# Performance work log

Hardware: AMD Instinct MI355X
Metric: run time of the kernel (lower is better)

Reference implementation:

```python
import jax, jax.numpy as jnp
import numpy as np

B, S, C = 4, 2048, 1024
E, H = 1024, 16
D = E // H  # head_dim = 64


def setup_inputs() -> dict:
    key = jax.random.key(0)
    k1, k2, k3, k4, k5 = jax.random.split(key, 5)
    s = 1.0 / np.sqrt(C)
    return {
        "x": jax.random.normal(k1, (B, S, C), dtype=jnp.float32),
        "w_qkv": jax.random.uniform(k2, (C, 3 * E), minval=-s, maxval=s, dtype=jnp.float32),
        "b_qkv": jax.random.uniform(k3, (3 * E,), minval=-s, maxval=s, dtype=jnp.float32),
        "w_out": jax.random.uniform(k4, (E, E), minval=-1.0 / np.sqrt(E), maxval=1.0 / np.sqrt(E), dtype=jnp.float32),
        "b_out": jax.random.uniform(k5, (E,), minval=-1.0 / np.sqrt(E), maxval=1.0 / np.sqrt(E), dtype=jnp.float32),
    }


def reference(x, w_qkv, b_qkv, w_out, b_out):
    b, s, _ = x.shape
    qkv = x @ w_qkv + b_qkv                      # [B,S,3E]
    qkv = qkv.reshape(b, s, 3, H, D)
    q = qkv[:, :, 0].transpose(0, 2, 1, 3)       # [B,H,S,D]
    k = qkv[:, :, 1].transpose(0, 2, 1, 3)
    v = qkv[:, :, 2].transpose(0, 2, 1, 3)
    scale = jnp.asarray(D, x.dtype) ** 0.5
    scores = jnp.einsum("bhqd,bhkd->bhqk", q, k) / scale
    attn = jax.nn.softmax(scores, axis=-1)       # dropout is identity in eval mode
    out = jnp.einsum("bhqk,bhkd->bhqd", attn, v)
    out = out.transpose(0, 2, 1, 3).reshape(b, s, E)
    return out @ w_out + b_out
```

## Files before the change

kernel.cpp:

```cpp
#include <hip/hip_runtime.h>


typedef _Float16 f16;
typedef f16 f16x2 __attribute__((ext_vector_type(2)));
typedef f16 f16x4 __attribute__((ext_vector_type(4)));
typedef f16 f16x8 __attribute__((ext_vector_type(8)));
typedef float f32x4 __attribute__((ext_vector_type(4)));

typedef const __attribute__((address_space(1))) void* gas_ptr;
typedef __attribute__((address_space(3))) void* lds_ptr;

__device__ __forceinline__ void load_lds16(const void* g, void* s) {
  __builtin_amdgcn_global_load_lds((gas_ptr)g, (lds_ptr)s, 16, 0, 0);
}

__device__ __forceinline__ f32x4 mfma16(f16x8 a, f16x8 b, f32x4 c) {
  return __builtin_amdgcn_mfma_f32_16x16x32_f16(a, b, c, 0, 0, 0);
}

__device__ __forceinline__ f32x4 mfma16k16(f16x4 a, f16x4 b, f32x4 c) {
  return __builtin_amdgcn_mfma_f32_16x16x16f16(a, b, c, 0, 0, 0);
}

__device__ __forceinline__ f16x2 pk2(float a, float b) {
  return __builtin_bit_cast(f16x2, __builtin_amdgcn_cvt_pkrtz(a, b));
}

__global__ __launch_bounds__(256) void cvt_x(const float* __restrict__ in, f16* __restrict__ out) {
  int i = blockIdx.x * 256 + threadIdx.x;
  const float4* p = (const float4*)in;
  float4 a = p[2 * i], b = p[2 * i + 1];
  f16x8 o;
  o[0] = (f16)a.x; o[1] = (f16)a.y; o[2] = (f16)a.z; o[3] = (f16)a.w;
  o[4] = (f16)b.x; o[5] = (f16)b.y; o[6] = (f16)b.z; o[7] = (f16)b.w;
  *(f16x8*)(out + 8 * (long)i) = o;
}

__global__ __launch_bounds__(256) void tconv(const float* __restrict__ in, f16* __restrict__ out,
                                             int R, int C) {
  __shared__ float t[32][33];
  int c0 = blockIdx.x * 32, r0 = blockIdx.y * 32;
  int tx = threadIdx.x, ty = threadIdx.y;
#pragma unroll
  for (int j = 0; j < 4; ++j)
    t[ty + 8 * j][tx] = in[(long)(r0 + ty + 8 * j) * C + c0 + tx];
  __syncthreads();
#pragma unroll
  for (int j = 0; j < 4; ++j)
    out[(long)(c0 + ty + 8 * j) * R + r0 + tx] = (f16)t[tx][ty + 8 * j];
}

__global__ __launch_bounds__(256) void qkv_gemm(const f16* __restrict__ A, const f16* __restrict__ BT,
                                                const float* __restrict__ bias,
                                                f16* __restrict__ Qs, f16* __restrict__ Kk,
                                                f16* __restrict__ Vt) {
  __shared__ __align__(16) f16 lA[128 * 32];
  __shared__ __align__(16) f16 lB[128 * 32];
  const int K = 1024;
  int tid = threadIdx.x, w = tid >> 6, lane = tid & 63, l16 = lane & 15, quad = lane >> 4;
  int wm = (w >> 1) * 64, wn = (w & 1) * 64;
  int blockM = blockIdx.x * 128, blockN = blockIdx.y * 128;
  f32x4 acc[4][4] = {};

  for (int k0 = 0; k0 < K; k0 += 32) {
    __syncthreads();
#pragma unroll
    for (int i = 0; i < 2; ++i) {
      int c = (i * 4 + w) * 64 + lane;
      load_lds16(A + (blockM + (c >> 2)) * K + k0 + (c & 3) * 8, lA + (i * 4 + w) * 512);
      load_lds16(BT + (blockN + (c >> 2)) * K + k0 + (c & 3) * 8, lB + (i * 4 + w) * 512);
    }
    __syncthreads();
    f16x8 af[4], bf[4];
#pragma unroll
    for (int mb = 0; mb < 4; ++mb) af[mb] = *(const f16x8*)&lA[(wm + mb * 16 + l16) * 32 + quad * 8];
#pragma unroll
    for (int nb = 0; nb < 4; ++nb) bf[nb] = *(const f16x8*)&lB[(wn + nb * 16 + l16) * 32 + quad * 8];
#pragma unroll
    for (int mb = 0; mb < 4; ++mb)
#pragma unroll
      for (int nb = 0; nb < 4; ++nb)
        acc[mb][nb] = mfma16(af[mb], bf[nb], acc[mb][nb]);
  }

  int which = blockIdx.y >> 3;
  const float SCALE = 0.18033688011112042f;
#pragma unroll
  for (int nb = 0; nb < 4; ++nb) {
    int col = blockN + wn + nb * 16 + l16;
    int hd = col & 1023, h = hd >> 6, d = hd & 63;
    float bv = bias[col];
#pragma unroll
    for (int mb = 0; mb < 4; ++mb) {
      int row0 = blockM + wm + mb * 16 + quad * 4;
      int b = row0 >> 11, s0 = row0 & 2047;
      if (which == 2) {
        f16x2 a = pk2(acc[mb][nb][0] + bv, acc[mb][nb][1] + bv);
        f16x2 c = pk2(acc[mb][nb][2] + bv, acc[mb][nb][3] + bv);
        *(f16x4*)&Vt[((b * 16 + h) * 64 + d) * 2048 + s0] =
            __builtin_shufflevector(a, c, 0, 1, 2, 3);
      } else if (which == 0) {
#pragma unroll
        for (int r = 0; r < 4; ++r)
          Qs[((b * 16 + h) * 2048 + s0 + r) * 64 + d] = (f16)((acc[mb][nb][r] + bv) * SCALE);
      } else {
#pragma unroll
        for (int r = 0; r < 4; ++r)
          Kk[((b * 16 + h) * 2048 + s0 + r) * 64 + d] = (f16)(acc[mb][nb][r] + bv);
      }
    }
  }
}

__global__ __launch_bounds__(256) void attn(const f16* __restrict__ Qs, const f16* __restrict__ Kk,
                                            const f16* __restrict__ Vt, f16* __restrict__ ctx) {
  __shared__ __align__(16) f16 lK[2][64 * 72];
  __shared__ __align__(16) f16 lV[2][64 * 72];
  int qt = blockIdx.x, bh = blockIdx.y;
  int tid = threadIdx.x, lane = tid & 63, l16 = lane & 15, quad = lane >> 4;
  int w = tid >> 6;
  const f16* Qbase = Qs + ((long)bh * 2048 + qt * 256 + w * 64) * 64;
  const f16* Kbh = Kk + (long)bh * 2048 * 64;
  const f16* Vbh = Vt + (long)bh * 64 * 2048;

  f16x8 qf[4][2];
#pragma unroll
  for (int rb = 0; rb < 4; ++rb)
#pragma unroll
    for (int ks = 0; ks < 2; ++ks)
      qf[rb][ks] = *(const f16x8*)(Qbase + (rb * 16 + l16) * 64 + ks * 32 + quad * 8);

  f32x4 of[4][4] = {};
  f32x4 osum[4] = {};
  const f16 one = (f16)1.f;
  const f16x4 vone = {one, one, one, one};

  int c0 = tid, c1 = 256 + tid;
  int r0s = c0 >> 3, o0 = (c0 & 7) * 8;
  int r1s = c1 >> 3, o1 = (c1 & 7) * 8;

  *(float4*)&lK[0][r0s * 72 + o0] = *(const float4*)(Kbh + r0s * 64 + o0);
  *(float4*)&lK[0][r1s * 72 + o1] = *(const float4*)(Kbh + r1s * 64 + o1);
  *(float4*)&lV[0][r0s * 72 + o0] = *(const float4*)(Vbh + (long)r0s * 2048 + o0);
  *(float4*)&lV[0][r1s * 72 + o1] = *(const float4*)(Vbh + (long)r1s * 2048 + o1);
  __syncthreads();

  for (int kt = 0; kt < 32; ++kt) {
    int cur = kt & 1, nxt = cur ^ 1;

    float4 pk0, pk1, pv0, pv1;
    if (kt < 31) {
      int kb0 = (kt + 1) * 64;
      pk0 = *(const float4*)(Kbh + (kb0 + r0s) * 64 + o0);
      pk1 = *(const float4*)(Kbh + (kb0 + r1s) * 64 + o1);
      pv0 = *(const float4*)(Vbh + (long)r0s * 2048 + kb0 + o0);
      pv1 = *(const float4*)(Vbh + (long)r1s * 2048 + kb0 + o1);
    }

#pragma unroll
    for (int kb = 0; kb < 4; ++kb) {
      f16x8 kf0 = *(const f16x8*)&lK[cur][(kb * 16 + l16) * 72 + quad * 8];
      f16x8 kf1 = *(const f16x8*)&lK[cur][(kb * 16 + l16) * 72 + 32 + quad * 8];

      f16x4 pa[4];
#pragma unroll
      for (int rb = 0; rb < 4; ++rb) {
        f32x4 z = {};
        z = mfma16(kf0, qf[rb][0], z);
        z = mfma16(kf1, qf[rb][1], z);
        float p0 = __builtin_amdgcn_exp2f(z[0]);
        float p1 = __builtin_amdgcn_exp2f(z[1]);
        float p2 = __builtin_amdgcn_exp2f(z[2]);
        float p3 = __builtin_amdgcn_exp2f(z[3]);
        pa[rb] = __builtin_shufflevector(pk2(p0, p1), pk2(p2, p3), 0, 1, 2, 3);
      }

#pragma unroll
      for (int db = 0; db < 4; ++db) {
        f16x4 vf = *(const f16x4*)&lV[cur][(db * 16 + l16) * 72 + kb * 16 + quad * 4];
#pragma unroll
        for (int rb = 0; rb < 4; ++rb)
          of[rb][db] = mfma16k16(pa[rb], vf, of[rb][db]);
      }
#pragma unroll
      for (int rb = 0; rb < 4; ++rb)
        osum[rb] = mfma16k16(pa[rb], vone, osum[rb]);
    }

    if (kt < 31) {
      *(float4*)&lK[nxt][r0s * 72 + o0] = pk0;
      *(float4*)&lK[nxt][r1s * 72 + o1] = pk1;
      *(float4*)&lV[nxt][r0s * 72 + o0] = pv0;
      *(float4*)&lV[nxt][r1s * 72 + o1] = pv1;
      __syncthreads();
    }
  }

  int b = bh >> 4, h = bh & 15;
  long token0 = (long)b * 2048 + qt * 256 + w * 64;
#pragma unroll
  for (int rb = 0; rb < 4; ++rb) {
    float inv[4];
#pragma unroll
    for (int r = 0; r < 4; ++r) inv[r] = 1.0f / osum[rb][r];
#pragma unroll
    for (int db = 0; db < 4; ++db)
#pragma unroll
      for (int r = 0; r < 4; ++r)
        ctx[(token0 + rb * 16 + quad * 4 + r) * 1024 + h * 64 + db * 16 + l16] =
            (f16)(of[rb][db][r] * inv[r]);
  }
}

__global__ __launch_bounds__(256) void proj_gemm(const f16* __restrict__ A, const f16* __restrict__ BT,
                                                 const float* __restrict__ bias,
                                                 float* __restrict__ out) {
  __shared__ __align__(16) f16 lA[128 * 32];
  __shared__ __align__(16) f16 lB[128 * 32];
  const int K = 1024;
  int tid = threadIdx.x, w = tid >> 6, lane = tid & 63, l16 = lane & 15, quad = lane >> 4;
  int wm = (w >> 1) * 64, wn = (w & 1) * 64;
  int blockM = blockIdx.x * 128, blockN = blockIdx.y * 128;
  f32x4 acc[4][4] = {};

  for (int k0 = 0; k0 < K; k0 += 32) {
    __syncthreads();
#pragma unroll
    for (int i = 0; i < 2; ++i) {
      int c = (i * 4 + w) * 64 + lane;
      load_lds16(A + (blockM + (c >> 2)) * K + k0 + (c & 3) * 8, lA + (i * 4 + w) * 512);
      load_lds16(BT + (blockN + (c >> 2)) * K + k0 + (c & 3) * 8, lB + (i * 4 + w) * 512);
    }
    __syncthreads();
    f16x8 af[4], bf[4];
#pragma unroll
    for (int mb = 0; mb < 4; ++mb) af[mb] = *(const f16x8*)&lA[(wm + mb * 16 + l16) * 32 + quad * 8];
#pragma unroll
    for (int nb = 0; nb < 4; ++nb) bf[nb] = *(const f16x8*)&lB[(wn + nb * 16 + l16) * 32 + quad * 8];
#pragma unroll
    for (int mb = 0; mb < 4; ++mb)
#pragma unroll
      for (int nb = 0; nb < 4; ++nb)
        acc[mb][nb] = mfma16(af[mb], bf[nb], acc[mb][nb]);
  }

#pragma unroll
  for (int nb = 0; nb < 4; ++nb) {
    int col = blockN + wn + nb * 16 + l16;
    float bv = bias[col];
#pragma unroll
    for (int mb = 0; mb < 4; ++mb) {
#pragma unroll
      for (int r = 0; r < 4; ++r) {
        int row = blockM + wm + mb * 16 + quad * 4 + r;
        out[(long)row * 1024 + col] = acc[mb][nb][r] + bv;
      }
    }
  }
}

extern "C" void kernel_launch(void* const* d_in, const int* in_sizes, int n_in,
                              void* d_out, int out_size, void* d_ws, size_t ws_size,
                              hipStream_t stream) {
  const float* x     = (const float*)d_in[0];
  const float* w_qkv = (const float*)d_in[1];
  const float* b_qkv = (const float*)d_in[2];
  const float* w_out = (const float*)d_in[3];
  const float* b_out = (const float*)d_in[4];
  float* out = (float*)d_out;

  char* ws = (char*)d_ws;
  f16* xh    = (f16*)(ws);
  f16* ctx   = (f16*)(ws);
  f16* wqkvT = (f16*)(ws + 16777216);
  f16* woutT = (f16*)(ws + 23068672);
  f16* Qs    = (f16*)(ws + 25165824);
  f16* Kk    = (f16*)(ws + 41943040);
  f16* Vt    = (f16*)(ws + 58720256);

  cvt_x<<<4096, 256, 0, stream>>>(x, xh);
  tconv<<<dim3(96, 32), dim3(32, 8), 0, stream>>>(w_qkv, wqkvT, 1024, 3072);
  tconv<<<dim3(32, 32), dim3(32, 8), 0, stream>>>(w_out, woutT, 1024, 1024);
  qkv_gemm<<<dim3(64, 24), 256, 0, stream>>>(xh, wqkvT, b_qkv, Qs, Kk, Vt);
  attn<<<dim3(8, 64), 256, 0, stream>>>(Qs, Kk, Vt, ctx);
  proj_gemm<<<dim3(64, 8), 256, 0, stream>>>(ctx, woutT, b_out, out);
}
```

Before: 278.9 us.

## Read K and V tiles directly from global memory instead of LDS staging

Removes the double-buffered LDS staging of K and V tiles in the attention kernel, along with its __syncthreads barriers. Each wave now loads its MFMA operands straight from global memory, relying on L1/L2 caching since the four waves of a block read the same K/V data. This drops LDS traffic and synchronization but gives up explicit prefetch overlap and causes redundant global loads across waves, with smaller per-lane vector loads for V.

```diff
diff --git a/kernel.cpp b/kernel.cpp
--- a/kernel.cpp
+++ b/kernel.cpp
@@ -114,8 +114,6 @@
 
 __global__ __launch_bounds__(256) void attn(const f16* __restrict__ Qs, const f16* __restrict__ Kk,
                                             const f16* __restrict__ Vt, f16* __restrict__ ctx) {
-  __shared__ __align__(16) f16 lK[2][64 * 72];
-  __shared__ __align__(16) f16 lV[2][64 * 72];
   int qt = blockIdx.x, bh = blockIdx.y;
   int tid = threadIdx.x, lane = tid & 63, l16 = lane & 15, quad = lane >> 4;
   int w = tid >> 6;
@@ -135,32 +133,13 @@
   const f16 one = (f16)1.f;
   const f16x4 vone = {one, one, one, one};
 
-  int c0 = tid, c1 = 256 + tid;
-  int r0s = c0 >> 3, o0 = (c0 & 7) * 8;
-  int r1s = c1 >> 3, o1 = (c1 & 7) * 8;
-
-  *(float4*)&lK[0][r0s * 72 + o0] = *(const float4*)(Kbh + r0s * 64 + o0);
-  *(float4*)&lK[0][r1s * 72 + o1] = *(const float4*)(Kbh + r1s * 64 + o1);
-  *(float4*)&lV[0][r0s * 72 + o0] = *(const float4*)(Vbh + (long)r0s * 2048 + o0);
-  *(float4*)&lV[0][r1s * 72 + o1] = *(const float4*)(Vbh + (long)r1s * 2048 + o1);
-  __syncthreads();
-
   for (int kt = 0; kt < 32; ++kt) {
-    int cur = kt & 1, nxt = cur ^ 1;
-
-    float4 pk0, pk1, pv0, pv1;
-    if (kt < 31) {
-      int kb0 = (kt + 1) * 64;
-      pk0 = *(const float4*)(Kbh + (kb0 + r0s) * 64 + o0);
-      pk1 = *(const float4*)(Kbh + (kb0 + r1s) * 64 + o1);
-      pv0 = *(const float4*)(Vbh + (long)r0s * 2048 + kb0 + o0);
-      pv1 = *(const float4*)(Vbh + (long)r1s * 2048 + kb0 + o1);
-    }
-
+    const f16* Kt = Kbh + kt * 64 * 64;
 #pragma unroll
     for (int kb = 0; kb < 4; ++kb) {
-      f16x8 kf0 = *(const f16x8*)&lK[cur][(kb * 16 + l16) * 72 + quad * 8];
-      f16x8 kf1 = *(const f16x8*)&lK[cur][(kb * 16 + l16) * 72 + 32 + quad * 8];
+      const f16* Krow = Kt + (kb * 16 + l16) * 64;
+      f16x8 kf0 = *(const f16x8*)(Krow + quad * 8);
+      f16x8 kf1 = *(const f16x8*)(Krow + 32 + quad * 8);
 
       f16x4 pa[4];
 #pragma unroll
@@ -175,9 +154,10 @@
         pa[rb] = __builtin_shufflevector(pk2(p0, p1), pk2(p2, p3), 0, 1, 2, 3);
       }
 
+      int vcol = kt * 64 + kb * 16 + quad * 4;
 #pragma unroll
       for (int db = 0; db < 4; ++db) {
-        f16x4 vf = *(const f16x4*)&lV[cur][(db * 16 + l16) * 72 + kb * 16 + quad * 4];
+        f16x4 vf = *(const f16x4*)&Vbh[(long)(db * 16 + l16) * 2048 + vcol];
 #pragma unroll
         for (int rb = 0; rb < 4; ++rb)
           of[rb][db] = mfma16k16(pa[rb], vf, of[rb][db]);
@@ -185,14 +165,6 @@
 #pragma unroll
       for (int rb = 0; rb < 4; ++rb)
         osum[rb] = mfma16k16(pa[rb], vone, osum[rb]);
-    }
-
-    if (kt < 31) {
-      *(float4*)&lK[nxt][r0s * 72 + o0] = pk0;
-      *(float4*)&lK[nxt][r1s * 72 + o1] = pk1;
-      *(float4*)&lV[nxt][r0s * 72 + o0] = pv0;
-      *(float4*)&lV[nxt][r1s * 72 + o1] = pv1;
-      __syncthreads();
     }
   }
 
```

Measured after the change: 375.1 us. 1.34x slower.
